# Kernel optimization log

Hardware: AMD Instinct MI355X
Metric: run time of the kernel (lower is better)

## Reference

```python
import jax, jax.numpy as jnp
import numpy as np

N_NODES = 100000
N_EDGES = 3200000
IN_DIM = 512
HID = 512
OUT_DIM = 256
BN_EPS = 1e-5


def setup_inputs() -> dict:
    key = jax.random.key(0)
    ks = jax.random.split(key, 16)
    x = jax.random.normal(ks[0], (N_NODES, IN_DIM), dtype=jnp.float32)
    adj_row = jax.random.randint(ks[1], (N_EDGES,), 0, N_NODES, dtype=jnp.int32)
    adj_col = jax.random.randint(ks[2], (N_EDGES,), 0, N_NODES, dtype=jnp.int32)
    adj_val = jax.random.uniform(ks[3], (N_EDGES,), dtype=jnp.float32)
    # GraphConvolution params (xavier_normal for weights, zero bias)
    def xavier(k, fan_in, fan_out):
        std = np.sqrt(2.0 / (fan_in + fan_out))
        return std * jax.random.normal(k, (fan_in, fan_out), dtype=jnp.float32)
    W1 = xavier(ks[4], IN_DIM, HID)
    b1 = jnp.zeros((HID,), jnp.float32)
    W2 = xavier(ks[5], HID, OUT_DIM)
    b2 = jnp.zeros((OUT_DIM,), jnp.float32)
    # BatchNorm affine params
    gamma1 = jnp.ones((HID,), jnp.float32)
    beta1 = jnp.zeros((HID,), jnp.float32)
    gamma2 = jnp.ones((OUT_DIM,), jnp.float32)
    beta2 = jnp.zeros((OUT_DIM,), jnp.float32)
    # Attention MLP: dim -> dim//4 -> dim (kaiming-uniform-ish init is fine for a reference)
    Wa1 = xavier(ks[6], HID, HID // 4)
    ba1 = jnp.zeros((HID // 4,), jnp.float32)
    Wa2 = xavier(ks[7], HID // 4, HID)
    ba2 = jnp.zeros((HID,), jnp.float32)
    return {
        "x": x, "adj_row": adj_row, "adj_col": adj_col, "adj_val": adj_val,
        "W1": W1, "b1": b1, "gamma1": gamma1, "beta1": beta1,
        "Wa1": Wa1, "ba1": ba1, "Wa2": Wa2, "ba2": ba2,
        "W2": W2, "b2": b2, "gamma2": gamma2, "beta2": beta2,
    }


def _gcn_layer(x, W, b, row, col, val, n_nodes):
    # support = x @ W ; out = sparse(adj) @ support + b ; gelu
    support = x @ W                                   # [N, F]
    gathered = val[:, None] * support[col]            # [E, F]
    out = jax.ops.segment_sum(gathered, row, num_segments=n_nodes) + b
    return jax.nn.gelu(out, approximate=False)


def _batchnorm(x, gamma, beta):
    # training-mode BatchNorm1d over nodes: biased variance, eps=1e-5
    mean = jnp.mean(x, axis=0)
    var = jnp.mean(jnp.square(x - mean), axis=0)
    return (x - mean) * jax.lax.rsqrt(var + BN_EPS) * gamma + beta


def reference(x, adj_row, adj_col, adj_val,
              W1, b1, gamma1, beta1,
              Wa1, ba1, Wa2, ba2,
              W2, b2, gamma2, beta2):
    n = x.shape[0]
    x1 = _gcn_layer(x, W1, b1, adj_row, adj_col, adj_val, n)
    x1 = _batchnorm(x1, gamma1, beta1)
    # dropout: eval mode (identity) for a deterministic reference
    attn = jax.nn.sigmoid(jax.nn.relu(x1 @ Wa1 + ba1) @ Wa2 + ba2)
    x1 = x1 * attn
    x2 = _gcn_layer(x1, W2, b2, adj_row, adj_col, adj_val, n)
    x2 = _batchnorm(x2, gamma2, beta2)
    return x2
```

## Files before the change

### kernel.cpp

```cpp
#include <hip/hip_runtime.h>
#include <cstdint>
#include <cstddef>

#define IN_DIM 512
#define HID 512
#define OUT_DIM 256
#define BN_EPS 1e-5f

typedef unsigned short u16;
typedef short s16x8 __attribute__((ext_vector_type(8)));
typedef float f32x4 __attribute__((ext_vector_type(4)));

__device__ __forceinline__ float gelu_f(float x) {
    return 0.5f * x * (1.0f + erff(x * 0.70710678118654752f));
}
__device__ __forceinline__ float bflo(uint32_t p) {
    uint32_t t = p << 16; float f; __builtin_memcpy(&f, &t, 4); return f;
}
__device__ __forceinline__ float bfhi(uint32_t p) {
    uint32_t t = p & 0xffff0000u; float f; __builtin_memcpy(&f, &t, 4); return f;
}
__device__ __forceinline__ float bfu(u16 u) {
    uint32_t t = (uint32_t)u << 16; float f; __builtin_memcpy(&f, &t, 4); return f;
}
__device__ __forceinline__ u16 f2bf(float f) {
    uint32_t x; __builtin_memcpy(&x, &f, 4);
    uint32_t r = x + 0x7fffu + ((x >> 16) & 1u);
    return (u16)(r >> 16);
}
__device__ __forceinline__ void gld_lds16(void* lds, const void* gp) {
    __builtin_amdgcn_global_load_lds(
        (const __attribute__((address_space(1))) void*)gp,
        (__attribute__((address_space(3))) void*)lds, 16, 0, 0);
}

__global__ void zero_kernel(int* __restrict__ p, int n) {
    int i = blockIdx.x * 256 + threadIdx.x;
    if (i < n) p[i] = 0;
}

__global__ void count_edges(const int* __restrict__ row, int ne, int* __restrict__ counts) {
    int e = blockIdx.x * 256 + threadIdx.x;
    if (e < ne) atomicAdd(&counts[row[e]], 1);
}

template<int BS>
__global__ void scan_block(const int* __restrict__ in, int n,
                           int* __restrict__ out, int* __restrict__ bsums) {
    __shared__ int tmp[BS];
    int t = threadIdx.x;
    int gid = blockIdx.x * BS + t;
    int v = (gid < n) ? in[gid] : 0;
    tmp[t] = v;
    __syncthreads();
    for (int off = 1; off < BS; off <<= 1) {
        int add = (t >= off) ? tmp[t - off] : 0;
        __syncthreads();
        tmp[t] += add;
        __syncthreads();
    }
    if (gid < n) out[gid] = tmp[t] - v;
    if (t == BS - 1 && bsums) bsums[blockIdx.x] = tmp[t];
}

__global__ void scan_add(int* __restrict__ row_start, int* __restrict__ cur_off,
                         const int* __restrict__ bsums, int n) {
    int gid = blockIdx.x * 256 + threadIdx.x;
    if (gid < n) {
        int v = row_start[gid] + bsums[blockIdx.x];
        row_start[gid] = v;
        cur_off[gid] = v;
    }
}

__global__ void scatter_edges(const int* __restrict__ row, const int* __restrict__ col,
                              const float* __restrict__ val, int ne,
                              int* __restrict__ cur_off, int2* __restrict__ epk) {
    int e = blockIdx.x * 256 + threadIdx.x;
    if (e < ne) {
        int r = row[e];
        int p = atomicAdd(&cur_off[r], 1);
        epk[p] = make_int2(col[e], __float_as_int(val[e]));
    }
}

__global__ __launch_bounds__(256) void cast_to_bf16(const float* __restrict__ in,
                                                    u16* __restrict__ out, size_t n) {
    size_t base = ((size_t)blockIdx.x * 256 + threadIdx.x) * 8;
    if (base >= n) return;
    float4 a = *(const float4*)(in + base);
    float4 b = *(const float4*)(in + base + 4);
    u16 o[8] = {f2bf(a.x), f2bf(a.y), f2bf(a.z), f2bf(a.w),
                f2bf(b.x), f2bf(b.y), f2bf(b.z), f2bf(b.w)};
    uint4 pk; __builtin_memcpy(&pk, o, 16);
    *(uint4*)(out + base) = pk;
}

__global__ __launch_bounds__(256) void transpose_cast(const float* __restrict__ in,
                                                      u16* __restrict__ out, int K, int N) {
    __shared__ float t[32][33];
    int tx = threadIdx.x & 31, ty = threadIdx.x >> 5;
    int k0 = blockIdx.x * 32, n0 = blockIdx.y * 32;
#pragma unroll
    for (int i = ty; i < 32; i += 8) t[i][tx] = in[(size_t)(k0 + i) * N + n0 + tx];
    __syncthreads();
#pragma unroll
    for (int i = ty; i < 32; i += 8) out[(size_t)(n0 + i) * K + k0 + tx] = f2bf(t[tx][i]);
}

template<int EPI>
__global__ __launch_bounds__(256) void gemm_bt(
    const u16* __restrict__ A, const u16* __restrict__ Bt,
    u16* __restrict__ C, const float* __restrict__ bias,
    const u16* __restrict__ extra, int M, int N, int K)
{
    __shared__ u16 Alds[128 * 32];
    __shared__ u16 Blds[128 * 32];
    const int tid = threadIdx.x;
    const int wid = tid >> 6, lane = tid & 63;
    const int wm = wid >> 1, wn = wid & 1;
    const int row0 = blockIdx.x * 128, col0 = blockIdx.y * 128;
    const int srow = lane >> 2;
    const int scol = (lane & 3) * 8;
    const int fr = lane & 15;
    const int fk = (lane >> 4) * 8;

    f32x4 acc[4][4];
#pragma unroll
    for (int i = 0; i < 4; ++i)
#pragma unroll
        for (int j = 0; j < 4; ++j) acc[i][j] = f32x4{0.f, 0.f, 0.f, 0.f};

    for (int k0 = 0; k0 < K; k0 += 32) {
#pragma unroll
        for (int c = 0; c < 2; ++c) {
            int tr = wid * 32 + c * 16 + srow;
            int ar = row0 + tr; if (ar >= M) ar = M - 1;
            gld_lds16(&Alds[(wid * 32 + c * 16) * 32], A + (size_t)ar * K + k0 + scol);
            gld_lds16(&Blds[(wid * 32 + c * 16) * 32], Bt + (size_t)(col0 + tr) * K + k0 + scol);
        }
        __syncthreads();
        s16x8 af[4], bfv[4];
#pragma unroll
        for (int m = 0; m < 4; ++m)
            af[m] = *(const s16x8*)&Alds[(wm * 64 + m * 16 + fr) * 32 + fk];
#pragma unroll
        for (int n = 0; n < 4; ++n)
            bfv[n] = *(const s16x8*)&Blds[(wn * 64 + n * 16 + fr) * 32 + fk];
#pragma unroll
        for (int m = 0; m < 4; ++m)
#pragma unroll
            for (int n = 0; n < 4; ++n)
                acc[m][n] = __builtin_amdgcn_mfma_f32_16x16x32_bf16(af[m], bfv[n], acc[m][n], 0, 0, 0);
        __syncthreads();
    }

#pragma unroll
    for (int n = 0; n < 4; ++n) {
        const int c = col0 + wn * 64 + n * 16 + fr;
        float bv = 0.f;
        if (EPI != 0) bv = bias[c];
#pragma unroll
        for (int m = 0; m < 4; ++m) {
            const int rbase = row0 + wm * 64 + m * 16 + (lane >> 4) * 4;
#pragma unroll
            for (int q = 0; q < 4; ++q) {
                int rr = rbase + q;
                if (rr < M) {
                    float v = acc[m][n][q];
                    if (EPI == 1) v = fmaxf(v + bv, 0.f);
                    else if (EPI == 2) {
                        float ev = bfu(extra[(size_t)rr * N + c]);
                        v = ev / (1.f + expf(-(v + bv)));
                    }
                    C[(size_t)rr * N + c] = f2bf(v);
                }
            }
        }
    }
}

template<int F, bool OUTBF>
__global__ __launch_bounds__(F / 2) void spmm_bg(
    const u16* __restrict__ sup, const int2* __restrict__ epk,
    const int* __restrict__ row_start, const int* __restrict__ counts,
    const float* __restrict__ bias, float* __restrict__ outf,
    u16* __restrict__ outb, int n)
{
    const int row = blockIdx.x;
    const int tid = threadIdx.x;
    const int start = row_start[row];
    const int nnz = counts[row];
    const uint32_t* supu = (const uint32_t*)sup;
    float a0 = 0.f, a1 = 0.f;
    int j = 0;
    for (; j + 1 < nnz; j += 2) {
        int2 e0 = epk[start + j], e1 = epk[start + j + 1];
        uint32_t p0 = supu[(size_t)e0.x * (F / 2) + tid];
        uint32_t p1 = supu[(size_t)e1.x * (F / 2) + tid];
        float v0 = __int_as_float(e0.y), v1 = __int_as_float(e1.y);
        a0 = fmaf(v0, bflo(p0), a0); a1 = fmaf(v0, bfhi(p0), a1);
        a0 = fmaf(v1, bflo(p1), a0); a1 = fmaf(v1, bfhi(p1), a1);
    }
    if (j < nnz) {
        int2 e = epk[start + j];
        uint32_t p = supu[(size_t)e.x * (F / 2) + tid];
        float v = __int_as_float(e.y);
        a0 = fmaf(v, bflo(p), a0); a1 = fmaf(v, bfhi(p), a1);
    }
    float o0 = gelu_f(a0 + bias[2 * tid]);
    float o1 = gelu_f(a1 + bias[2 * tid + 1]);
    if (OUTBF) {
        uint32_t pk = (uint32_t)f2bf(o0) | ((uint32_t)f2bf(o1) << 16);
        ((uint32_t*)outb)[(size_t)row * (F / 2) + tid] = pk;
    } else {
        *(float2*)&outf[(size_t)row * F + 2 * tid] = make_float2(o0, o1);
    }
}

template<int F>
__global__ __launch_bounds__(256) void bn_reduce_bf16(const u16* __restrict__ x, int n,
                                                      float* __restrict__ ssum,
                                                      float* __restrict__ ssq) {
    const int tid = threadIdx.x;
    int r0 = blockIdx.x * 256, rend = min(r0 + 256, n);
    const uint32_t* xu = (const uint32_t*)x;
    float s0 = 0, s1 = 0, q0 = 0, q1 = 0;
    for (int r = r0; r < rend; ++r) {
        uint32_t p = xu[(size_t)r * (F / 2) + tid];
        float v0 = bflo(p), v1 = bfhi(p);
        s0 += v0; q0 += v0 * v0;
        s1 += v1; q1 += v1 * v1;
    }
    atomicAdd(&ssum[2 * tid], s0);     atomicAdd(&ssum[2 * tid + 1], s1);
    atomicAdd(&ssq[2 * tid], q0);      atomicAdd(&ssq[2 * tid + 1], q1);
}

template<int F>
__global__ __launch_bounds__(256) void bn_apply_bf16(u16* __restrict__ x, int n,
                                                     const float* __restrict__ ssum,
                                                     const float* __restrict__ ssq,
                                                     const float* __restrict__ gamma,
                                                     const float* __restrict__ beta) {
    float inv_n = 1.0f / (float)n;
    size_t total = (size_t)n * (F / 2);
    uint32_t* xu = (uint32_t*)x;
    for (size_t i = (size_t)blockIdx.x * 256 + threadIdx.x; i < total;
         i += (size_t)gridDim.x * 256) {
        int f0 = (int)((i * 2) & (size_t)(F - 1));
        uint32_t p = xu[i];
        float m0 = ssum[f0] * inv_n, m1 = ssum[f0 + 1] * inv_n;
        float sc0 = rsqrtf(ssq[f0] * inv_n - m0 * m0 + BN_EPS) * gamma[f0];
        float sc1 = rsqrtf(ssq[f0 + 1] * inv_n - m1 * m1 + BN_EPS) * gamma[f0 + 1];
        float v0 = (bflo(p) - m0) * sc0 + beta[f0];
        float v1 = (bfhi(p) - m1) * sc1 + beta[f0 + 1];
        xu[i] = (uint32_t)f2bf(v0) | ((uint32_t)f2bf(v1) << 16);
    }
}

template<int F>
__global__ __launch_bounds__(256) void bn_reduce(const float* __restrict__ x, int n,
                                                 float* __restrict__ ssum, float* __restrict__ ssq) {
    constexpr int NV = F / 256;
    int tid = threadIdx.x;
    int r0 = blockIdx.x * 256, rend = min(r0 + 256, n);
    float s[NV] = {}, q[NV] = {};
    for (int r = r0; r < rend; ++r) {
#pragma unroll
        for (int k = 0; k < NV; ++k) {
            float v = x[(size_t)r * F + tid + k * 256];
            s[k] += v; q[k] += v * v;
        }
    }
#pragma unroll
    for (int k = 0; k < NV; ++k) {
        atomicAdd(&ssum[tid + k * 256], s[k]);
        atomicAdd(&ssq[tid + k * 256], q[k]);
    }
}

template<int F>
__global__ __launch_bounds__(256) void bn_apply(float* __restrict__ x, int n,
                                                const float* __restrict__ ssum,
                                                const float* __restrict__ ssq,
                                                const float* __restrict__ gamma,
                                                const float* __restrict__ beta) {
    float inv_n = 1.0f / (float)n;
    size_t total4 = (size_t)n * F / 4;
    for (size_t i = (size_t)blockIdx.x * 256 + threadIdx.x; i < total4;
         i += (size_t)gridDim.x * 256) {
        float4 v = ((const float4*)x)[i];
        int f0 = (int)((i * 4) & (size_t)(F - 1));
        float in[4] = {v.x, v.y, v.z, v.w};
#pragma unroll
        for (int k = 0; k < 4; ++k) {
            int f = f0 + k;
            float mean = ssum[f] * inv_n;
            float var = ssq[f] * inv_n - mean * mean;
            float sc = rsqrtf(var + BN_EPS) * gamma[f];
            in[k] = (in[k] - mean) * sc + beta[f];
        }
        v.x = in[0]; v.y = in[1]; v.z = in[2]; v.w = in[3];
        ((float4*)x)[i] = v;
    }
}

extern "C" void kernel_launch(void* const* d_in, const int* in_sizes, int n_in,
                              void* d_out, int out_size, void* d_ws, size_t ws_size,
                              hipStream_t stream) {
    const float* x       = (const float*)d_in[0];
    const int*   adj_row = (const int*)d_in[1];
    const int*   adj_col = (const int*)d_in[2];
    const float* adj_val = (const float*)d_in[3];
    const float* W1      = (const float*)d_in[4];
    const float* b1      = (const float*)d_in[5];
    const float* gamma1  = (const float*)d_in[6];
    const float* beta1   = (const float*)d_in[7];
    const float* Wa1     = (const float*)d_in[8];
    const float* ba1     = (const float*)d_in[9];
    const float* Wa2     = (const float*)d_in[10];
    const float* ba2     = (const float*)d_in[11];
    const float* W2      = (const float*)d_in[12];
    const float* b2      = (const float*)d_in[13];
    const float* gamma2  = (const float*)d_in[14];
    const float* beta2   = (const float*)d_in[15];

    const int N = in_sizes[0] / IN_DIM;
    const int E = in_sizes[1];

    char* ws = (char*)d_ws;
    size_t off = 0;
    auto alloc = [&](size_t bytes) -> void* {
        void* p = ws + off;
        off = (off + bytes + 255) & ~(size_t)255;
        return p;
    };
    u16*  x16    = (u16*)alloc((size_t)N * IN_DIM * 2);
    u16*  sup16  = (u16*)alloc((size_t)N * HID * 2);
    u16*  x1_16  = (u16*)alloc((size_t)N * HID * 2);
    u16*  h16    = (u16*)alloc((size_t)N * (HID / 4) * 2);
    int2* epk    = (int2*)alloc((size_t)E * 8);
    int*  counts = (int*)alloc((size_t)N * 4);
    int*  row_st = (int*)alloc((size_t)N * 4);
    int*  cur_of = (int*)alloc((size_t)N * 4);
    int*  bsums  = (int*)alloc(4096);
    float* stats = (float*)alloc(1536 * 4);
    u16*  W1t    = (u16*)alloc(512 * 512 * 2);
    u16*  Wa1t   = (u16*)alloc(128 * 512 * 2);
    u16*  Wa2t   = (u16*)alloc(512 * 128 * 2);
    u16*  W2t    = (u16*)alloc(256 * 512 * 2);
    float* ssum1 = stats, *ssq1 = stats + 512, *ssum2 = stats + 1024, *ssq2 = stats + 1280;
    u16*  gated16 = x16;

    const int nb_n = (N + 255) / 256;
    const int nb_e = (E + 255) / 256;
    const int gm = (N + 127) / 128;

    zero_kernel<<<nb_n, 256, 0, stream>>>(counts, N);
    zero_kernel<<<6, 256, 0, stream>>>((int*)stats, 1536);
    count_edges<<<nb_e, 256, 0, stream>>>(adj_row, E, counts);
    scan_block<256><<<nb_n, 256, 0, stream>>>(counts, N, row_st, bsums);
    scan_block<512><<<1, 512, 0, stream>>>(bsums, nb_n, bsums, nullptr);
    scan_add<<<nb_n, 256, 0, stream>>>(row_st, cur_of, bsums, N);
    scatter_edges<<<nb_e, 256, 0, stream>>>(adj_row, adj_col, adj_val, E, cur_of, epk);

    cast_to_bf16<<<(int)(((size_t)N * IN_DIM + 2047) / 2048), 256, 0, stream>>>(x, x16, (size_t)N * IN_DIM);
    transpose_cast<<<dim3(16, 16), 256, 0, stream>>>(W1, W1t, IN_DIM, HID);
    transpose_cast<<<dim3(16, 4), 256, 0, stream>>>(Wa1, Wa1t, HID, HID / 4);
    transpose_cast<<<dim3(4, 16), 256, 0, stream>>>(Wa2, Wa2t, HID / 4, HID);
    transpose_cast<<<dim3(16, 8), 256, 0, stream>>>(W2, W2t, HID, OUT_DIM);

    gemm_bt<0><<<dim3(gm, HID / 128), 256, 0, stream>>>(x16, W1t, sup16, nullptr, nullptr, N, HID, IN_DIM);
    spmm_bg<HID, true><<<N, HID / 2, 0, stream>>>(sup16, epk, row_st, counts, b1, nullptr, x1_16, N);
    bn_reduce_bf16<HID><<<nb_n, 256, 0, stream>>>(x1_16, N, ssum1, ssq1);
    bn_apply_bf16<HID><<<2048, 256, 0, stream>>>(x1_16, N, ssum1, ssq1, gamma1, beta1);

    gemm_bt<1><<<dim3(gm, 1), 256, 0, stream>>>(x1_16, Wa1t, h16, ba1, nullptr, N, HID / 4, HID);
    gemm_bt<2><<<dim3(gm, HID / 128), 256, 0, stream>>>(h16, Wa2t, gated16, ba2, x1_16, N, HID, HID / 4);

    gemm_bt<0><<<dim3(gm, OUT_DIM / 128), 256, 0, stream>>>(gated16, W2t, sup16, nullptr, nullptr, N, OUT_DIM, HID);
    spmm_bg<OUT_DIM, false><<<N, OUT_DIM / 2, 0, stream>>>(sup16, epk, row_st, counts, b2, (float*)d_out, nullptr, N);
    bn_reduce<OUT_DIM><<<nb_n, 256, 0, stream>>>((float*)d_out, N, ssum2, ssq2);
    bn_apply<OUT_DIM><<<2048, 256, 0, stream>>>((float*)d_out, N, ssum2, ssq2, gamma2, beta2);
}
```

Measured before the change: 2.144 ms.

## Fold BatchNorm into attention GEMM weights and use wave-per-row SpMM

Removes the bn_apply pass over the hidden activations. The BN scale is folded into the columns of the transposed Wa1 weights and the BN shift into a precomputed bias. The BN affine is also applied inside the gating GEMM epilogue when reading x1. Separately, the SpMM is rewritten so each 64-lane wave handles one row, using vectorized 8- or 16-byte loads and unrolling edges by four. Folding BN scaling into bf16 weights adds an extra rounding step that could slightly change numerics.

New measurement: 2.202 ms. 1.03x slower.

```diff
diff --git a/kernel.cpp b/kernel.cpp
--- a/kernel.cpp
+++ b/kernel.cpp
@@ -108,11 +108,45 @@
     for (int i = ty; i < 32; i += 8) out[(size_t)(n0 + i) * K + k0 + tx] = f2bf(t[tx][i]);
 }
 
+__global__ void bn_coeffs(const float* __restrict__ ssum, const float* __restrict__ ssq,
+                          const float* __restrict__ gamma, const float* __restrict__ beta,
+                          float* __restrict__ s, float* __restrict__ t, int F, float inv_n) {
+    int f = blockIdx.x * 256 + threadIdx.x;
+    if (f < F) {
+        float m = ssum[f] * inv_n;
+        float var = ssq[f] * inv_n - m * m;
+        float sc = rsqrtf(var + BN_EPS) * gamma[f];
+        s[f] = sc;
+        t[f] = beta[f] - m * sc;
+    }
+}
+
+__global__ __launch_bounds__(256) void scale_cols_bf16(u16* __restrict__ W,
+                                                       const float* __restrict__ s,
+                                                       int total, int K) {
+    int idx = blockIdx.x * 256 + threadIdx.x;
+    if (idx < total) {
+        int k = idx & (K - 1);
+        W[idx] = f2bf(bfu(W[idx]) * s[k]);
+    }
+}
+
+__global__ void fold_bias(const float* __restrict__ Wa1, const float* __restrict__ ba,
+                          const float* __restrict__ t, float* __restrict__ biasp,
+                          int K, int Nout) {
+    int n = threadIdx.x;
+    if (n >= Nout) return;
+    float acc = ba[n];
+    for (int k = 0; k < K; ++k) acc = fmaf(t[k], Wa1[(size_t)k * Nout + n], acc);
+    biasp[n] = acc;
+}
+
 template<int EPI>
 __global__ __launch_bounds__(256) void gemm_bt(
     const u16* __restrict__ A, const u16* __restrict__ Bt,
     u16* __restrict__ C, const float* __restrict__ bias,
-    const u16* __restrict__ extra, int M, int N, int K)
+    const u16* __restrict__ extra, const float* __restrict__ gs,
+    const float* __restrict__ gt, int M, int N, int K)
 {
     __shared__ u16 Alds[128 * 32];
     __shared__ u16 Blds[128 * 32];
@@ -158,8 +192,9 @@
 #pragma unroll
     for (int n = 0; n < 4; ++n) {
         const int c = col0 + wn * 64 + n * 16 + fr;
-        float bv = 0.f;
+        float bv = 0.f, sv = 0.f, tv = 0.f;
         if (EPI != 0) bv = bias[c];
+        if (EPI == 2) { sv = gs[c]; tv = gt[c]; }
 #pragma unroll
         for (int m = 0; m < 4; ++m) {
             const int rbase = row0 + wm * 64 + m * 16 + (lane >> 4) * 4;
@@ -170,7 +205,7 @@
                     float v = acc[m][n][q];
                     if (EPI == 1) v = fmaxf(v + bv, 0.f);
                     else if (EPI == 2) {
-                        float ev = bfu(extra[(size_t)rr * N + c]);
+                        float ev = bfu(extra[(size_t)rr * N + c]) * sv + tv;
                         v = ev / (1.f + expf(-(v + bv)));
                     }
                     C[(size_t)rr * N + c] = f2bf(v);
@@ -181,40 +216,92 @@
 }
 
 template<int F, bool OUTBF>
-__global__ __launch_bounds__(F / 2) void spmm_bg(
+__global__ __launch_bounds__(256) void spmm_wave(
     const u16* __restrict__ sup, const int2* __restrict__ epk,
     const int* __restrict__ row_start, const int* __restrict__ counts,
     const float* __restrict__ bias, float* __restrict__ outf,
     u16* __restrict__ outb, int n)
 {
-    const int row = blockIdx.x;
-    const int tid = threadIdx.x;
+    constexpr int WPR = F / 128;
+    constexpr int FPL = 2 * WPR;
+    const int lane = threadIdx.x & 63;
+    const int row = blockIdx.x * 4 + (threadIdx.x >> 6);
+    if (row >= n) return;
     const int start = row_start[row];
     const int nnz = counts[row];
     const uint32_t* supu = (const uint32_t*)sup;
-    float a0 = 0.f, a1 = 0.f;
+    const size_t lbase = (size_t)lane * WPR;
+
+    float acc[FPL];
+#pragma unroll
+    for (int k = 0; k < FPL; ++k) acc[k] = 0.f;
+
     int j = 0;
-    for (; j + 1 < nnz; j += 2) {
-        int2 e0 = epk[start + j], e1 = epk[start + j + 1];
-        uint32_t p0 = supu[(size_t)e0.x * (F / 2) + tid];
-        uint32_t p1 = supu[(size_t)e1.x * (F / 2) + tid];
-        float v0 = __int_as_float(e0.y), v1 = __int_as_float(e1.y);
-        a0 = fmaf(v0, bflo(p0), a0); a1 = fmaf(v0, bfhi(p0), a1);
-        a0 = fmaf(v1, bflo(p1), a0); a1 = fmaf(v1, bfhi(p1), a1);
-    }
-    if (j < nnz) {
+    for (; j + 4 <= nnz; j += 4) {
+        int2 e[4];
+#pragma unroll
+        for (int u = 0; u < 4; ++u) e[u] = epk[start + j + u];
+#pragma unroll
+        for (int u = 0; u < 4; ++u) {
+            const uint32_t* p = &supu[(size_t)e[u].x * (F / 2) + lbase];
+            float v = __int_as_float(e[u].y);
+            if (WPR == 4) {
+                uint4 q = *(const uint4*)p;
+                acc[0] = fmaf(v, bflo(q.x), acc[0]); acc[1] = fmaf(v, bfhi(q.x), acc[1]);
+                acc[2] = fmaf(v, bflo(q.y), acc[2]); acc[3] = fmaf(v, bfhi(q.y), acc[3]);
+                acc[4] = fmaf(v, bflo(q.z), acc[4]); acc[5] = fmaf(v, bfhi(q.z), acc[5]);
+                acc[6] = fmaf(v, bflo(q.w), acc[6]); acc[7] = fmaf(v, bfhi(q.w), acc[7]);
+            } else {
+                uint2 q = *(const uint2*)p;
+                acc[0] = fmaf(v, bflo(q.x), acc[0]); acc[1] = fmaf(v, bfhi(q.x), acc[1]);
+                acc[2] = fmaf(v, bflo(q.y), acc[2]); acc[3] = fmaf(v, bfhi(q.y), acc[3]);
+            }
+        }
+    }
+    for (; j < nnz; ++j) {
         int2 e = epk[start + j];
-        uint32_t p = supu[(size_t)e.x * (F / 2) + tid];
+        const uint32_t* p = &supu[(size_t)e.x * (F / 2) + lbase];
         float v = __int_as_float(e.y);
-        a0 = fmaf(v, bflo(p), a0); a1 = fmaf(v, bfhi(p), a1);
-    }
-    float o0 = gelu_f(a0 + bias[2 * tid]);
-    float o1 = gelu_f(a1 + bias[2 * tid + 1]);
+        if (WPR == 4) {
+            uint4 q = *(const uint4*)p;
+            acc[0] = fmaf(v, bflo(q.x), acc[0]); acc[1] = fmaf(v, bfhi(q.x), acc[1]);
+            acc[2] = fmaf(v, bflo(q.y), acc[2]); acc[3] = fmaf(v, bfhi(q.y), acc[3]);
+            acc[4] = fmaf(v, bflo(q.z), acc[4]); acc[5] = fmaf(v, bfhi(q.z), acc[5]);
+            acc[6] = fmaf(v, bflo(q.w), acc[6]); acc[7] = fmaf(v, bfhi(q.w), acc[7]);
+        } else {
+            uint2 q = *(const uint2*)p;
+            acc[0] = fmaf(v, bflo(q.x), acc[0]); acc[1] = fmaf(v, bfhi(q.x), acc[1]);
+            acc[2] = fmaf(v, bflo(q.y), acc[2]); acc[3] = fmaf(v, bfhi(q.y), acc[3]);
+        }
+    }
+
+    const int f0 = lane * FPL;
+    float o[FPL];
+#pragma unroll
+    for (int k = 0; k < FPL; ++k) o[k] = gelu_f(acc[k] + bias[f0 + k]);
+
     if (OUTBF) {
-        uint32_t pk = (uint32_t)f2bf(o0) | ((uint32_t)f2bf(o1) << 16);
-        ((uint32_t*)outb)[(size_t)row * (F / 2) + tid] = pk;
+        u16 pk[FPL];
+#pragma unroll
+        for (int k = 0; k < FPL; ++k) pk[k] = f2bf(o[k]);
+        if (WPR == 4) {
+            uint4 w; __builtin_memcpy(&w, pk, 16);
+            *(uint4*)&outb[(size_t)row * F + f0] = w;
+        } else {
+            uint2 w; __builtin_memcpy(&w, pk, 8);
+            *(uint2*)&outb[(size_t)row * F + f0] = w;
+        }
     } else {
-        *(float2*)&outf[(size_t)row * F + 2 * tid] = make_float2(o0, o1);
+        if (WPR == 2) {
+            float4 w = make_float4(o[0], o[1], o[2], o[3]);
+            *(float4*)&outf[(size_t)row * F + f0] = w;
+        } else {
+#pragma unroll
+            for (int k = 0; k < FPL; k += 4) {
+                float4 w = make_float4(o[k], o[k + 1], o[k + 2], o[k + 3]);
+                *(float4*)&outf[(size_t)row * F + f0 + k] = w;
+            }
+        }
     }
 }
 
@@ -234,28 +321,6 @@
     }
     atomicAdd(&ssum[2 * tid], s0);     atomicAdd(&ssum[2 * tid + 1], s1);
     atomicAdd(&ssq[2 * tid], q0);      atomicAdd(&ssq[2 * tid + 1], q1);
-}
-
-template<int F>
-__global__ __launch_bounds__(256) void bn_apply_bf16(u16* __restrict__ x, int n,
-                                                     const float* __restrict__ ssum,
-                                                     const float* __restrict__ ssq,
-                                                     const float* __restrict__ gamma,
-                                                     const float* __restrict__ beta) {
-    float inv_n = 1.0f / (float)n;
-    size_t total = (size_t)n * (F / 2);
-    uint32_t* xu = (uint32_t*)x;
-    for (size_t i = (size_t)blockIdx.x * 256 + threadIdx.x; i < total;
-         i += (size_t)gridDim.x * 256) {
-        int f0 = (int)((i * 2) & (size_t)(F - 1));
-        uint32_t p = xu[i];
-        float m0 = ssum[f0] * inv_n, m1 = ssum[f0 + 1] * inv_n;
-        float sc0 = rsqrtf(ssq[f0] * inv_n - m0 * m0 + BN_EPS) * gamma[f0];
-        float sc1 = rsqrtf(ssq[f0 + 1] * inv_n - m1 * m1 + BN_EPS) * gamma[f0 + 1];
-        float v0 = (bflo(p) - m0) * sc0 + beta[f0];
-        float v1 = (bfhi(p) - m1) * sc1 + beta[f0 + 1];
-        xu[i] = (uint32_t)f2bf(v0) | ((uint32_t)f2bf(v1) << 16);
-    }
 }
 
 template<int F>
@@ -345,6 +410,9 @@
     int*  cur_of = (int*)alloc((size_t)N * 4);
     int*  bsums  = (int*)alloc(4096);
     float* stats = (float*)alloc(1536 * 4);
+    float* s1    = (float*)alloc(512 * 4);
+    float* t1    = (float*)alloc(512 * 4);
+    float* bias1p= (float*)alloc(128 * 4);
     u16*  W1t    = (u16*)alloc(512 * 512 * 2);
     u16*  Wa1t   = (u16*)alloc(128 * 512 * 2);
     u16*  Wa2t   = (u16*)alloc(512 * 128 * 2);
@@ -355,6 +423,7 @@
     const int nb_n = (N + 255) / 256;
     const int nb_e = (E + 255) / 256;
     const int gm = (N + 127) / 128;
+    const int sg = (N + 3) / 4;
 
     zero_kernel<<<nb_n, 256, 0, stream>>>(counts, N);
     zero_kernel<<<6, 256, 0, stream>>>((int*)stats, 1536);
@@ -370,16 +439,18 @@
     transpose_cast<<<dim3(4, 16), 256, 0, stream>>>(Wa2, Wa2t, HID / 4, HID);
     transpose_cast<<<dim3(16, 8), 256, 0, stream>>>(W2, W2t, HID, OUT_DIM);
 
-    gemm_bt<0><<<dim3(gm, HID / 128), 256, 0, stream>>>(x16, W1t, sup16, nullptr, nullptr, N, HID, IN_DIM);
-    spmm_bg<HID, true><<<N, HID / 2, 0, stream>>>(sup16, epk, row_st, counts, b1, nullptr, x1_16, N);
+    gemm_bt<0><<<dim3(gm, HID / 128), 256, 0, stream>>>(x16, W1t, sup16, nullptr, nullptr, nullptr, nullptr, N, HID, IN_DIM);
+    spmm_wave<HID, true><<<sg, 256, 0, stream>>>(sup16, epk, row_st, counts, b1, nullptr, x1_16, N);
     bn_reduce_bf16<HID><<<nb_n, 256, 0, stream>>>(x1_16, N, ssum1, ssq1);
-    bn_apply_bf16<HID><<<2048, 256, 0, stream>>>(x1_16, N, ssum1, ssq1, gamma1, beta1);
-
-    gemm_bt<1><<<dim3(gm, 1), 256, 0, stream>>>(x1_16, Wa1t, h16, ba1, nullptr, N, HID / 4, HID);
-    gemm_bt<2><<<dim3(gm, HID / 128), 256, 0, stream>>>(h16, Wa2t, gated16, ba2, x1_16, N, HID, HID / 4);
-
-    gemm_bt<0><<<dim3(gm, OUT_DIM / 128), 256, 0, stream>>>(gated16, W2t, sup16, nullptr, nullptr, N, OUT_DIM, HID);
-    spmm_bg<OUT_DIM, false><<<N, OUT_DIM / 2, 0, stream>>>(sup16, epk, row_st, counts, b2, (float*)d_out, nullptr, N);
+    bn_coeffs<<<2, 256, 0, stream>>>(ssum1, ssq1, gamma1, beta1, s1, t1, HID, 1.0f / N);
+    scale_cols_bf16<<<(128 * 512) / 256, 256, 0, stream>>>(Wa1t, s1, 128 * 512, 512);
+    fold_bias<<<1, 128, 0, stream>>>(Wa1, ba1, t1, bias1p, HID, HID / 4);
+
+    gemm_bt<1><<<dim3(gm, 1), 256, 0, stream>>>(x1_16, Wa1t, h16, bias1p, nullptr, nullptr, nullptr, N, HID / 4, HID);
+    gemm_bt<2><<<dim3(gm, HID / 128), 256, 0, stream>>>(h16, Wa2t, gated16, ba2, x1_16, s1, t1, N, HID, HID / 4);
+
+    gemm_bt<0><<<dim3(gm, OUT_DIM / 128), 256, 0, stream>>>(gated16, W2t, sup16, nullptr, nullptr, nullptr, nullptr, N, OUT_DIM, HID);
+    spmm_wave<OUT_DIM, false><<<sg, 256, 0, stream>>>(sup16, epk, row_st, counts, b2, (float*)d_out, nullptr, N);
     bn_reduce<OUT_DIM><<<nb_n, 256, 0, stream>>>((float*)d_out, N, ssum2, ssq2);
     bn_apply<OUT_DIM><<<2048, 256, 0, stream>>>((float*)d_out, N, ssum2, ssq2, gamma2, beta2);
 }
```
